# Kernel optimization log

Measured on AMD Instinct MI355X. Metric: run time of the kernel, lower is better.

Reference implementation:

```python
import jax, jax.numpy as jnp
import numpy as np

UNI, HID, FLD = 512, 1024, 128
B, S = 128, 512

def setup_inputs() -> dict:
    key = jax.random.key(0)
    ks = jax.random.split(key, 8)
    input_embeddings = jax.random.normal(ks[0], (B, S, UNI), dtype=jnp.float32)
    field_embeddings = jax.random.normal(ks[1], (B, S, FLD), dtype=jnp.float32)
    input_length = jax.random.randint(ks[2], (B,), 1, S + 1)
    input_length = input_length.at[0].set(S)  # ensure loop runs full S steps -> static output shape
    s1 = 1.0 / np.sqrt(UNI + HID)
    s2 = 1.0 / np.sqrt(FLD)
    W1 = jax.random.uniform(ks[3], (4 * HID, UNI + HID), minval=-s1, maxval=s1, dtype=jnp.float32)
    b1 = jax.random.uniform(ks[4], (4 * HID,), minval=-s1, maxval=s1, dtype=jnp.float32)
    W2 = jax.random.uniform(ks[5], (2 * HID, FLD), minval=-s2, maxval=s2, dtype=jnp.float32)
    b2 = jax.random.uniform(ks[6], (2 * HID,), minval=-s2, maxval=s2, dtype=jnp.float32)
    return {"input_embeddings": input_embeddings, "field_embeddings": field_embeddings,
            "input_length": input_length, "W1": W1, "b1": b1, "W2": W2, "b2": b2}

def reference(input_embeddings, field_embeddings, input_length, W1, b1, W2, b2):
    Bc, Sc, _ = input_embeddings.shape
    H = W1.shape[0] // 4
    h0 = jnp.zeros((Bc, H), dtype=input_embeddings.dtype)
    c0 = jnp.zeros((Bc, H), dtype=input_embeddings.dtype)

    def step(carry, xs):
        h_prev, c_prev, t = carry
        x_t, f_t = xs
        fin = (t >= input_length)[:, None]  # [B,1] bool
        pre = jnp.concatenate([x_t, h_prev], axis=1) @ W1.T + b1  # [B,4H]
        i, j, f, o = jnp.split(pre, 4, axis=1)
        rd = f_t @ W2.T + b2  # [B,2H]
        r, d = jnp.split(rd, 2, axis=1)
        c = (jax.nn.sigmoid(f + 1.0) * c_prev
             + jax.nn.sigmoid(i) * jnp.tanh(j)
             + jax.nn.sigmoid(r) * jnp.tanh(d))
        h = jax.nn.sigmoid(o) * jnp.tanh(c)
        out = jnp.where(fin, 0.0, h)
        h_new = jnp.where(fin, h_prev, h)
        c_new = jnp.where(fin, c_prev, c)
        return (h_new, c_new, t + 1), out

    xs = (input_embeddings.transpose(1, 0, 2), field_embeddings.transpose(1, 0, 2))
    (h, c, _), outs = jax.lax.scan(step, (h0, c0, jnp.int32(0)), xs)
    return outs.transpose(1, 0, 2), (h, c)
```

## Files before the change

kernel.cpp:

```cpp
#include <hip/hip_runtime.h>
#include <cstdint>
#include <cstddef>


typedef __bf16 bf16;
typedef __bf16 bf16x8 __attribute__((ext_vector_type(8)));
typedef float floatx4 __attribute__((ext_vector_type(4)));

#define B_ 128
#define S_ 512
#define UNI_ 512
#define HID_ 1024
#define FLD_ 128
#define K1_ 1536
#define BS_STRIDE 1544

__device__ __forceinline__ float sigf(float x) { return 1.0f / (1.0f + __expf(-x)); }

__global__ __launch_bounds__(128) void sort_kernel(const int* __restrict__ len,
                                                   int* __restrict__ perm,
                                                   int* __restrict__ lens) {
  int i = threadIdx.x;
  int li = len[i];
  int r = 0;
  for (int j = 0; j < B_; ++j) {
    int lj = len[j];
    r += (lj > li) || (lj == li && j < i) ? 1 : 0;
  }
  perm[r] = i;
  lens[r] = li;
}

__global__ __launch_bounds__(256) void conv_w(const float* __restrict__ W1,
                                              const float* __restrict__ W2,
                                              bf16* __restrict__ W1b,
                                              bf16* __restrict__ W2b) {
  int i = blockIdx.x * 256 + threadIdx.x;
  if (i < 4096 * K1_) W1b[i] = (bf16)W1[i];
  else {
    int j = i - 4096 * K1_;
    if (j < 2048 * FLD_) W2b[j] = (bf16)W2[j];
  }
}

__global__ __launch_bounds__(256) void zero_state(bf16* __restrict__ h0,
                                                  bf16* __restrict__ h1,
                                                  float* __restrict__ c,
                                                  float* __restrict__ hf) {
  int i = blockIdx.x * 256 + threadIdx.x;
  h0[i] = (bf16)0.0f;
  h1[i] = (bf16)0.0f;
  c[i] = 0.0f;
  hf[i] = 0.0f;
}

__global__ __launch_bounds__(256) void conv_xf(const float* __restrict__ x,
                                               const float* __restrict__ f,
                                               const int* __restrict__ perm,
                                               bf16* __restrict__ xbf,
                                               bf16* __restrict__ fbf) {
  int t = blockIdx.x, rs = blockIdx.y, tid = threadIdx.x;
  int b = perm[rs];
  const float* xs = x + ((size_t)b * S_ + t) * UNI_;
  bf16* xd = xbf + ((size_t)rs * S_ + t) * UNI_;
  xd[tid] = (bf16)xs[tid];
  xd[tid + 256] = (bf16)xs[tid + 256];
  if (tid < FLD_) {
    fbf[((size_t)rs * S_ + t) * FLD_ + tid] =
        (bf16)f[((size_t)b * S_ + t) * FLD_ + tid];
  }
}

__global__ __launch_bounds__(256) void zero_tail(const int* __restrict__ len,
                                                 float* __restrict__ out) {
  int t = blockIdx.x, b = blockIdx.y;
  if (t < len[b]) return;
  float4 z = {0.0f, 0.0f, 0.0f, 0.0f};
  float4* o = (float4*)(out + ((size_t)b * S_ + t) * HID_);
  o[threadIdx.x] = z;
}

__global__ __launch_bounds__(512, 2) void step_kernel(
    const bf16* __restrict__ xbf,
    const bf16* __restrict__ fbf,
    const bf16* __restrict__ W1b,
    const bf16* __restrict__ W2b,
    const float* __restrict__ bias1,
    const float* __restrict__ bias2,
    const bf16* __restrict__ h_cur,
    bf16* __restrict__ h_nxt,
    float* __restrict__ c_ws,
    float* __restrict__ hf,
    const int* __restrict__ perm_g,
    const int* __restrict__ lens_g,
    float* __restrict__ out, int t) {
  __shared__ bf16 Bs[16 * BS_STRIDE];
  __shared__ float pre_s[128][17];
  __shared__ float rd_s[128][9];
  __shared__ int lens_s[128];
  __shared__ int perm_s[128];

  const int tid = threadIdx.x;
  const int nb = blockIdx.x;
  const int c0 = nb * 4;

  {
    const int n = tid >> 5;
    const int s = tid & 31;
    const int wrow = (n >> 2) * HID_ + c0 + (n & 3);
    const bf16* src = W1b + (size_t)wrow * K1_;
    bf16* dst = Bs + n * BS_STRIDE;
#pragma unroll
    for (int p = 0; p < 6; ++p) {
      int off = (p * 32 + s) * 8;
      *(bf16x8*)(dst + off) = *(const bf16x8*)(src + off);
    }
  }
  if (tid < 128) {
    lens_s[tid] = lens_g[tid];
    perm_s[tid] = perm_g[tid];
  }
  __syncthreads();

  const int wave = tid >> 6;
  const int lane = tid & 63;
  const int quad = lane >> 4;
  const int l16 = lane & 15;
  const int m = wave * 16 + l16;
  const int kq = quad * 8;

  const bool wave_active = (t < lens_s[wave * 16]);

  if (wave_active) {
    floatx4 acc_a = {0.f, 0.f, 0.f, 0.f};
    floatx4 acc_b = {0.f, 0.f, 0.f, 0.f};
    floatx4 accr = {0.f, 0.f, 0.f, 0.f};
    const bf16* xrow = xbf + ((size_t)m * S_ + t) * UNI_ + kq;
    const bf16* hrow = h_cur + (size_t)m * HID_ + kq;
    const bf16* bsl = Bs + l16 * BS_STRIDE + kq;

#pragma unroll
    for (int kc = 0; kc < UNI_; kc += 64) {
      bf16x8 a0 = *(const bf16x8*)(xrow + kc);
      bf16x8 b0 = *(const bf16x8*)(bsl + kc);
      bf16x8 a1 = *(const bf16x8*)(xrow + kc + 32);
      bf16x8 b1 = *(const bf16x8*)(bsl + kc + 32);
      acc_a = __builtin_amdgcn_mfma_f32_16x16x32_bf16(a0, b0, acc_a, 0, 0, 0);
      acc_b = __builtin_amdgcn_mfma_f32_16x16x32_bf16(a1, b1, acc_b, 0, 0, 0);
    }
#pragma unroll 8
    for (int kc = 0; kc < HID_; kc += 64) {
      bf16x8 a0 = *(const bf16x8*)(hrow + kc);
      bf16x8 b0 = *(const bf16x8*)(bsl + UNI_ + kc);
      bf16x8 a1 = *(const bf16x8*)(hrow + kc + 32);
      bf16x8 b1 = *(const bf16x8*)(bsl + UNI_ + kc + 32);
      acc_a = __builtin_amdgcn_mfma_f32_16x16x32_bf16(a0, b0, acc_a, 0, 0, 0);
      acc_b = __builtin_amdgcn_mfma_f32_16x16x32_bf16(a1, b1, acc_b, 0, 0, 0);
    }
    {
      const bf16* frow = fbf + ((size_t)m * S_ + t) * FLD_ + kq;
      const int w2row = ((l16 >> 2) & 1) * HID_ + c0 + (l16 & 3);
      const bf16* w2p = W2b + (size_t)w2row * FLD_ + kq;
#pragma unroll
      for (int kc = 0; kc < FLD_; kc += 32) {
        bf16x8 a0 = *(const bf16x8*)(frow + kc);
        bf16x8 b0 = *(const bf16x8*)(w2p + kc);
        accr = __builtin_amdgcn_mfma_f32_16x16x32_bf16(a0, b0, accr, 0, 0, 0);
      }
    }
    const int row0 = wave * 16 + quad * 4;
#pragma unroll
    for (int r = 0; r < 4; ++r) {
      pre_s[row0 + r][l16] = acc_a[r] + acc_b[r];
      if (l16 < 8) rd_s[row0 + r][l16] = accr[r];
    }
  }
  __syncthreads();

  {
    const int row = tid >> 2;
    const int cc = tid & 3;
    const int col = c0 + cc;
    const size_t sidx = (size_t)row * HID_ + col;
    if (t >= lens_s[row]) {
      h_nxt[sidx] = h_cur[sidx];
    } else {
      float iv = pre_s[row][cc] + bias1[col];
      float jv = pre_s[row][4 + cc] + bias1[HID_ + col];
      float fv = pre_s[row][8 + cc] + bias1[2 * HID_ + col];
      float ov = pre_s[row][12 + cc] + bias1[3 * HID_ + col];
      float rv = rd_s[row][cc] + bias2[col];
      float dv = rd_s[row][4 + cc] + bias2[HID_ + col];
      float cp = c_ws[sidx];
      float cn = sigf(fv + 1.0f) * cp + sigf(iv) * tanhf(jv) + sigf(rv) * tanhf(dv);
      float hn = sigf(ov) * tanhf(cn);
      out[(size_t)perm_s[row] * (S_ * HID_) + (size_t)t * HID_ + col] = hn;
      h_nxt[sidx] = (bf16)hn;
      c_ws[sidx] = cn;
      hf[sidx] = hn;
    }
  }
}

__global__ __launch_bounds__(256) void final_kernel(const float* __restrict__ hf,
                                                    const float* __restrict__ c,
                                                    const int* __restrict__ perm,
                                                    float* __restrict__ out) {
  int i = blockIdx.x * 256 + threadIdx.x;
  int rs = i >> 10, n = i & 1023;
  int b = perm[rs];
  const size_t base = (size_t)B_ * S_ * HID_;
  out[base + (size_t)b * HID_ + n] = hf[i];
  out[base + (size_t)B_ * HID_ + (size_t)b * HID_ + n] = c[i];
}

extern "C" void kernel_launch(void* const* d_in, const int* in_sizes, int n_in,
                              void* d_out, int out_size, void* d_ws, size_t ws_size,
                              hipStream_t stream) {
  const float* x = (const float*)d_in[0];
  const float* f = (const float*)d_in[1];
  const int* len = (const int*)d_in[2];
  const float* W1 = (const float*)d_in[3];
  const float* b1 = (const float*)d_in[4];
  const float* W2 = (const float*)d_in[5];
  const float* b2 = (const float*)d_in[6];
  float* out = (float*)d_out;

  char* ws = (char*)d_ws;
  bf16* W1b = (bf16*)(ws);
  bf16* W2b = (bf16*)(ws + 12582912);
  bf16* xbf = (bf16*)(ws + 13107200);
  bf16* fbf = (bf16*)(ws + 80216064);
  bf16* h0 = (bf16*)(ws + 96993280);
  bf16* h1 = (bf16*)(ws + 97255424);
  float* c = (float*)(ws + 97517568);
  float* hf = (float*)(ws + 98041856);
  int* perm = (int*)(ws + 98566144);
  int* lens = (int*)(ws + 98566656);

  sort_kernel<<<1, 128, 0, stream>>>(len, perm, lens);
  conv_w<<<(4096 * K1_ + 2048 * FLD_ + 255) / 256, 256, 0, stream>>>(W1, W2, W1b, W2b);
  zero_state<<<512, 256, 0, stream>>>(h0, h1, c, hf);
  conv_xf<<<dim3(S_, B_), 256, 0, stream>>>(x, f, perm, xbf, fbf);
  zero_tail<<<dim3(S_, B_), 256, 0, stream>>>(len, out);

  for (int t = 0; t < S_; ++t) {
    const bf16* hc = (t & 1) ? h1 : h0;
    bf16* hn = (t & 1) ? h0 : h1;
    step_kernel<<<256, 512, 0, stream>>>(xbf, fbf, W1b, W2b, b1, b2, hc, hn, c,
                                         hf, perm, lens, out, t);
  }

  final_kernel<<<512, 256, 0, stream>>>(hf, c, perm, out);
}
```

Baseline: 7.850 ms.

## Replace per-step kernel launches with a persistent kernel and grid barrier

Fuses the 512 per-timestep launches and the final copy kernel into one persistent kernel of 256 blocks that loops over time and synchronises through an atomic counter with a multi-slot spin barrier. The c and h state now stay in registers instead of global memory, W2 is staged once into LDS, and the x/f bf16 buffers are laid out time-major for contiguous per-step reads. This removes launch overhead and the cost of reloading the 48KB W1 slice into LDS at every step. It relies on all 256 blocks being co-resident for the spin barrier to avoid deadlock.

```diff
diff --git a/kernel.cpp b/kernel.cpp
--- a/kernel.cpp
+++ b/kernel.cpp
@@ -14,6 +14,8 @@
 #define FLD_ 128
 #define K1_ 1536
 #define BS_STRIDE 1544
+#define NBLK 256
+#define NSLOT 64
 
 __device__ __forceinline__ float sigf(float x) { return 1.0f / (1.0f + __expf(-x)); }
 
@@ -45,13 +47,11 @@
 
 __global__ __launch_bounds__(256) void zero_state(bf16* __restrict__ h0,
                                                   bf16* __restrict__ h1,
-                                                  float* __restrict__ c,
-                                                  float* __restrict__ hf) {
+                                                  int* __restrict__ bar) {
   int i = blockIdx.x * 256 + threadIdx.x;
   h0[i] = (bf16)0.0f;
   h1[i] = (bf16)0.0f;
-  c[i] = 0.0f;
-  hf[i] = 0.0f;
+  if (i < 32 + NSLOT * 32) bar[i] = 0;
 }
 
 __global__ __launch_bounds__(256) void conv_xf(const float* __restrict__ x,
@@ -62,11 +62,11 @@
   int t = blockIdx.x, rs = blockIdx.y, tid = threadIdx.x;
   int b = perm[rs];
   const float* xs = x + ((size_t)b * S_ + t) * UNI_;
-  bf16* xd = xbf + ((size_t)rs * S_ + t) * UNI_;
+  bf16* xd = xbf + ((size_t)t * B_ + rs) * UNI_;
   xd[tid] = (bf16)xs[tid];
   xd[tid + 256] = (bf16)xs[tid + 256];
   if (tid < FLD_) {
-    fbf[((size_t)rs * S_ + t) * FLD_ + tid] =
+    fbf[((size_t)t * B_ + rs) * FLD_ + tid] =
         (bf16)f[((size_t)b * S_ + t) * FLD_ + tid];
   }
 }
@@ -80,21 +80,48 @@
   o[threadIdx.x] = z;
 }
 
-__global__ __launch_bounds__(512, 2) void step_kernel(
+__device__ __forceinline__ void grid_barrier(int* __restrict__ bar, int t) {
+  __syncthreads();
+  if (threadIdx.x == 0) {
+    int* cnt = bar;
+    int* slots = bar + 32;
+    __threadfence();
+    int prev = __hip_atomic_fetch_add(cnt, 1, __ATOMIC_RELAXED,
+                                      __HIP_MEMORY_SCOPE_AGENT);
+    if (prev == NBLK - 1) {
+      __threadfence();
+      __hip_atomic_store(cnt, 0, __ATOMIC_RELAXED, __HIP_MEMORY_SCOPE_AGENT);
+      __threadfence();
+#pragma unroll
+      for (int s = 0; s < NSLOT; ++s)
+        __hip_atomic_store(&slots[s * 32], t + 1, __ATOMIC_RELAXED,
+                           __HIP_MEMORY_SCOPE_AGENT);
+    } else {
+      int* my = &slots[(blockIdx.x & (NSLOT - 1)) * 32];
+      while (__hip_atomic_load(my, __ATOMIC_RELAXED,
+                               __HIP_MEMORY_SCOPE_AGENT) <= t)
+        __builtin_amdgcn_s_sleep(2);
+      __threadfence();
+    }
+  }
+  __syncthreads();
+}
+
+__global__ __launch_bounds__(512, 2) void lstm_persistent(
     const bf16* __restrict__ xbf,
     const bf16* __restrict__ fbf,
     const bf16* __restrict__ W1b,
     const bf16* __restrict__ W2b,
     const float* __restrict__ bias1,
     const float* __restrict__ bias2,
-    const bf16* __restrict__ h_cur,
-    bf16* __restrict__ h_nxt,
-    float* __restrict__ c_ws,
-    float* __restrict__ hf,
+    bf16* __restrict__ ha,
+    bf16* __restrict__ hb,
     const int* __restrict__ perm_g,
     const int* __restrict__ lens_g,
-    float* __restrict__ out, int t) {
+    float* __restrict__ out,
+    int* __restrict__ bar) {
   __shared__ bf16 Bs[16 * BS_STRIDE];
+  __shared__ bf16 Ws2[8 * 136];
   __shared__ float pre_s[128][17];
   __shared__ float rd_s[128][9];
   __shared__ int lens_s[128];
@@ -120,6 +147,13 @@
     lens_s[tid] = lens_g[tid];
     perm_s[tid] = perm_g[tid];
   }
+  if (tid >= 128 && tid < 256) {
+    int q = tid - 128;
+    int r = q >> 4, s = q & 15;
+    int w2row = (r >> 2) * HID_ + c0 + (r & 3);
+    *(bf16x8*)(Ws2 + r * 136 + s * 8) =
+        *(const bf16x8*)(W2b + (size_t)w2row * FLD_ + s * 8);
+  }
   __syncthreads();
 
   const int wave = tid >> 6;
@@ -128,90 +162,95 @@
   const int l16 = lane & 15;
   const int m = wave * 16 + l16;
   const int kq = quad * 8;
-
-  const bool wave_active = (t < lens_s[wave * 16]);
-
-  if (wave_active) {
-    floatx4 acc_a = {0.f, 0.f, 0.f, 0.f};
-    floatx4 acc_b = {0.f, 0.f, 0.f, 0.f};
-    floatx4 accr = {0.f, 0.f, 0.f, 0.f};
-    const bf16* xrow = xbf + ((size_t)m * S_ + t) * UNI_ + kq;
-    const bf16* hrow = h_cur + (size_t)m * HID_ + kq;
-    const bf16* bsl = Bs + l16 * BS_STRIDE + kq;
-
-#pragma unroll
-    for (int kc = 0; kc < UNI_; kc += 64) {
-      bf16x8 a0 = *(const bf16x8*)(xrow + kc);
-      bf16x8 b0 = *(const bf16x8*)(bsl + kc);
-      bf16x8 a1 = *(const bf16x8*)(xrow + kc + 32);
-      bf16x8 b1 = *(const bf16x8*)(bsl + kc + 32);
-      acc_a = __builtin_amdgcn_mfma_f32_16x16x32_bf16(a0, b0, acc_a, 0, 0, 0);
-      acc_b = __builtin_amdgcn_mfma_f32_16x16x32_bf16(a1, b1, acc_b, 0, 0, 0);
-    }
+  const bf16* bsl = Bs + l16 * BS_STRIDE + kq;
+  const bf16* ws2p = Ws2 + ((((l16 >> 2) & 1) * 4 + (l16 & 3)) * 136) + kq;
+  const int wlen = lens_s[wave * 16];
+
+  const int urow = tid >> 2;
+  const int ucc = tid & 3;
+  const int ucol = c0 + ucc;
+  const float b1i = bias1[ucol];
+  const float b1j = bias1[HID_ + ucol];
+  const float b1f = bias1[2 * HID_ + ucol];
+  const float b1o = bias1[3 * HID_ + ucol];
+  const float b2r = bias2[ucol];
+  const float b2d = bias2[HID_ + ucol];
+  const int ulen = lens_s[urow];
+  const size_t hidx = (size_t)urow * HID_ + ucol;
+  float* outrow = out + (size_t)perm_s[urow] * (S_ * HID_) + ucol;
+
+  float c_my = 0.0f;
+  float h_my = 0.0f;
+
+  for (int t = 0; t < S_; ++t) {
+    const bf16* hcur = (t & 1) ? hb : ha;
+    bf16* hnxt = (t & 1) ? ha : hb;
+
+    if (t < wlen) {
+      floatx4 acc_a = {0.f, 0.f, 0.f, 0.f};
+      floatx4 acc_b = {0.f, 0.f, 0.f, 0.f};
+      floatx4 accr = {0.f, 0.f, 0.f, 0.f};
+      const bf16* xrow = xbf + ((size_t)t * B_ + m) * UNI_ + kq;
+      const bf16* hrow = hcur + (size_t)m * HID_ + kq;
+
+#pragma unroll
+      for (int kc = 0; kc < UNI_; kc += 64) {
+        bf16x8 a0 = *(const bf16x8*)(xrow + kc);
+        bf16x8 b0 = *(const bf16x8*)(bsl + kc);
+        bf16x8 a1 = *(const bf16x8*)(xrow + kc + 32);
+        bf16x8 b1 = *(const bf16x8*)(bsl + kc + 32);
+        acc_a = __builtin_amdgcn_mfma_f32_16x16x32_bf16(a0, b0, acc_a, 0, 0, 0);
+        acc_b = __builtin_amdgcn_mfma_f32_16x16x32_bf16(a1, b1, acc_b, 0, 0, 0);
+      }
 #pragma unroll 8
-    for (int kc = 0; kc < HID_; kc += 64) {
-      bf16x8 a0 = *(const bf16x8*)(hrow + kc);
-      bf16x8 b0 = *(const bf16x8*)(bsl + UNI_ + kc);
-      bf16x8 a1 = *(const bf16x8*)(hrow + kc + 32);
-      bf16x8 b1 = *(const bf16x8*)(bsl + UNI_ + kc + 32);
-      acc_a = __builtin_amdgcn_mfma_f32_16x16x32_bf16(a0, b0, acc_a, 0, 0, 0);
-      acc_b = __builtin_amdgcn_mfma_f32_16x16x32_bf16(a1, b1, acc_b, 0, 0, 0);
-    }
-    {
-      const bf16* frow = fbf + ((size_t)m * S_ + t) * FLD_ + kq;
-      const int w2row = ((l16 >> 2) & 1) * HID_ + c0 + (l16 & 3);
-      const bf16* w2p = W2b + (size_t)w2row * FLD_ + kq;
-#pragma unroll
-      for (int kc = 0; kc < FLD_; kc += 32) {
-        bf16x8 a0 = *(const bf16x8*)(frow + kc);
-        bf16x8 b0 = *(const bf16x8*)(w2p + kc);
-        accr = __builtin_amdgcn_mfma_f32_16x16x32_bf16(a0, b0, accr, 0, 0, 0);
-      }
-    }
-    const int row0 = wave * 16 + quad * 4;
-#pragma unroll
-    for (int r = 0; r < 4; ++r) {
-      pre_s[row0 + r][l16] = acc_a[r] + acc_b[r];
-      if (l16 < 8) rd_s[row0 + r][l16] = accr[r];
-    }
-  }
-  __syncthreads();
+      for (int kc = 0; kc < HID_; kc += 64) {
+        bf16x8 a0 = *(const bf16x8*)(hrow + kc);
+        bf16x8 b0 = *(const bf16x8*)(bsl + UNI_ + kc);
+        bf16x8 a1 = *(const bf16x8*)(hrow + kc + 32);
+        bf16x8 b1 = *(const bf16x8*)(bsl + UNI_ + kc + 32);
+        acc_a = __builtin_amdgcn_mfma_f32_16x16x32_bf16(a0, b0, acc_a, 0, 0, 0);
+        acc_b = __builtin_amdgcn_mfma_f32_16x16x32_bf16(a1, b1, acc_b, 0, 0, 0);
+      }
+      {
+        const bf16* frow = fbf + ((size_t)t * B_ + m) * FLD_ + kq;
+#pragma unroll
+        for (int kc = 0; kc < FLD_; kc += 32) {
+          bf16x8 a0 = *(const bf16x8*)(frow + kc);
+          bf16x8 b0 = *(const bf16x8*)(ws2p + kc);
+          accr = __builtin_amdgcn_mfma_f32_16x16x32_bf16(a0, b0, accr, 0, 0, 0);
+        }
+      }
+      const int row0 = wave * 16 + quad * 4;
+#pragma unroll
+      for (int r = 0; r < 4; ++r) {
+        pre_s[row0 + r][l16] = acc_a[r] + acc_b[r];
+        if (l16 < 8) rd_s[row0 + r][l16] = accr[r];
+      }
+    }
+    __syncthreads();
+
+    if (t < ulen) {
+      float iv = pre_s[urow][ucc] + b1i;
+      float jv = pre_s[urow][4 + ucc] + b1j;
+      float fv = pre_s[urow][8 + ucc] + b1f;
+      float ov = pre_s[urow][12 + ucc] + b1o;
+      float rv = rd_s[urow][ucc] + b2r;
+      float dv = rd_s[urow][4 + ucc] + b2d;
+      c_my = sigf(fv + 1.0f) * c_my + sigf(iv) * tanhf(jv) + sigf(rv) * tanhf(dv);
+      h_my = sigf(ov) * tanhf(c_my);
+      outrow[(size_t)t * HID_] = h_my;
+    }
+    hnxt[hidx] = (bf16)h_my;
+
+    grid_barrier(bar, t);
+  }
 
   {
-    const int row = tid >> 2;
-    const int cc = tid & 3;
-    const int col = c0 + cc;
-    const size_t sidx = (size_t)row * HID_ + col;
-    if (t >= lens_s[row]) {
-      h_nxt[sidx] = h_cur[sidx];
-    } else {
-      float iv = pre_s[row][cc] + bias1[col];
-      float jv = pre_s[row][4 + cc] + bias1[HID_ + col];
-      float fv = pre_s[row][8 + cc] + bias1[2 * HID_ + col];
-      float ov = pre_s[row][12 + cc] + bias1[3 * HID_ + col];
-      float rv = rd_s[row][cc] + bias2[col];
-      float dv = rd_s[row][4 + cc] + bias2[HID_ + col];
-      float cp = c_ws[sidx];
-      float cn = sigf(fv + 1.0f) * cp + sigf(iv) * tanhf(jv) + sigf(rv) * tanhf(dv);
-      float hn = sigf(ov) * tanhf(cn);
-      out[(size_t)perm_s[row] * (S_ * HID_) + (size_t)t * HID_ + col] = hn;
-      h_nxt[sidx] = (bf16)hn;
-      c_ws[sidx] = cn;
-      hf[sidx] = hn;
-    }
-  }
-}
-
-__global__ __launch_bounds__(256) void final_kernel(const float* __restrict__ hf,
-                                                    const float* __restrict__ c,
-                                                    const int* __restrict__ perm,
-                                                    float* __restrict__ out) {
-  int i = blockIdx.x * 256 + threadIdx.x;
-  int rs = i >> 10, n = i & 1023;
-  int b = perm[rs];
-  const size_t base = (size_t)B_ * S_ * HID_;
-  out[base + (size_t)b * HID_ + n] = hf[i];
-  out[base + (size_t)B_ * HID_ + (size_t)b * HID_ + n] = c[i];
+    const size_t base = (size_t)B_ * S_ * HID_;
+    const size_t prow = (size_t)perm_s[urow] * HID_ + ucol;
+    out[base + prow] = h_my;
+    out[base + (size_t)B_ * HID_ + prow] = c_my;
+  }
 }
 
 extern "C" void kernel_launch(void* const* d_in, const int* in_sizes, int n_in,
@@ -233,23 +272,16 @@
   bf16* fbf = (bf16*)(ws + 80216064);
   bf16* h0 = (bf16*)(ws + 96993280);
   bf16* h1 = (bf16*)(ws + 97255424);
-  float* c = (float*)(ws + 97517568);
-  float* hf = (float*)(ws + 98041856);
-  int* perm = (int*)(ws + 98566144);
-  int* lens = (int*)(ws + 98566656);
+  int* perm = (int*)(ws + 97517568);
+  int* lens = (int*)(ws + 97518080);
+  int* bar = (int*)(ws + 97518592);
 
   sort_kernel<<<1, 128, 0, stream>>>(len, perm, lens);
   conv_w<<<(4096 * K1_ + 2048 * FLD_ + 255) / 256, 256, 0, stream>>>(W1, W2, W1b, W2b);
-  zero_state<<<512, 256, 0, stream>>>(h0, h1, c, hf);
+  zero_state<<<512, 256, 0, stream>>>(h0, h1, bar);
   conv_xf<<<dim3(S_, B_), 256, 0, stream>>>(x, f, perm, xbf, fbf);
   zero_tail<<<dim3(S_, B_), 256, 0, stream>>>(len, out);
 
-  for (int t = 0; t < S_; ++t) {
-    const bf16* hc = (t & 1) ? h1 : h0;
-    bf16* hn = (t & 1) ? h0 : h1;
-    step_kernel<<<256, 512, 0, stream>>>(xbf, fbf, W1b, W2b, b1, b2, hc, hn, c,
-                                         hf, perm, lens, out, t);
-  }
-
-  final_kernel<<<512, 256, 0, stream>>>(hf, c, perm, out);
-}
+  lstm_persistent<<<NBLK, 512, 0, stream>>>(xbf, fbf, W1b, W2b, b1, b2, h0, h1,
+                                            perm, lens, out, bar);
+}
```

New measurement: 11.84 ms. 50.8% more time.
